# Optimization experiments

Measured on AMD Instinct MI355X. Metric: run time of the kernel, lower is better.

## Reference

```python
import jax, jax.numpy as jnp
import numpy as np

SR = 16000
HOP = 256
NH = 60
TWO_PI = 2.0 * np.pi


def _rescale(x):
    """Linear upsample along time (axis 1) by HOP, align_corners=True.
    x: [B, T, C] -> [B, T*HOP, C]. Matches F.interpolate(mode='linear', align_corners=True)."""
    T = x.shape[1]
    L = T * HOP
    pos = jnp.arange(L, dtype=jnp.float32) * (np.float32(T - 1) / np.float32(L - 1))
    i0 = jnp.clip(jnp.floor(pos).astype(jnp.int32), 0, T - 2)
    w = (pos - i0.astype(jnp.float32))[None, :, None]
    x0 = x[:, i0, :]
    x1 = x[:, i0 + 1, :]
    return x0 * (1.0 - w) + x1 * w


def setup_inputs() -> dict:
    key = jax.random.key(0)
    k1, k2, k3 = jax.random.split(key, 3)
    # fundamental frequency in a realistic 50-450 Hz range
    f0 = jax.random.uniform(k1, (8, 500, 1), dtype=jnp.float32) * 400.0 + 50.0
    loudness = jax.random.uniform(k2, (8, 500, 1), dtype=jnp.float32)
    harm_amps = jax.random.uniform(k3, (8, 500, NH), dtype=jnp.float32)
    return {"f0": f0, "loudness": loudness, "harm_amps": harm_amps}


def reference(f0, loudness, harm_amps):
    ks = jnp.arange(1, NH + 1, dtype=f0.dtype)          # harmonic numbers
    harmonics = f0 * ks                                  # [B,T,H] (einsum ijk,k->ijk with broadcast f0)
    harm_amps = jnp.where(harmonics > (SR // 2), 0.0, harm_amps)  # Nyquist mask
    harmonics = _rescale(harmonics * (TWO_PI / SR))      # [B, T*HOP, H] angular increments
    phases = jnp.mod(jnp.cumsum(harmonics, axis=1), TWO_PI)
    loud = _rescale(loudness)                            # [B, T*HOP, 1]
    amps = _rescale(harm_amps)                           # [B, T*HOP, H]
    signal = jnp.sum(loud * amps * jnp.sin(phases), axis=2)  # [B, T*HOP]
    return signal
```

## Files before the change

kernel.cpp:

```cpp
#include <hip/hip_runtime.h>
#include <hip/hip_bf16.h>


#define NHARM 60
#define TFRAMES 500
#define TM1 499
#define LOUT 128000
#define LM1U 127999u

__global__ __launch_bounds__(512) void osc_prefix_kernel(const float* __restrict__ f0,
                                                         double* __restrict__ H) {
    int b = blockIdx.x;
    int tid = threadIdx.x;
    double g = 0.0;
    if (tid < TM1) {
        unsigned t = (unsigned)tid;
        unsigned a   = (t * LM1U + 498u) / 499u;
        unsigned end = (t < TM1 - 1u) ? ((t + 1u) * LM1U + 498u) / 499u - 1u
                                      : LM1U;
        unsigned cnt   = end - a + 1u;
        unsigned rem_a = a * 499u - t * LM1U;
        unsigned num = cnt * rem_a + 499u * (cnt * (cnt - 1u) / 2u);
        double F = (double)num / 127999.0;
        double fa = (double)f0[b * TFRAMES + tid];
        double fb = (double)f0[b * TFRAMES + tid + 1];
        g = (double)cnt * fa + (fb - fa) * F;
    }
    __shared__ double sd[512];
    sd[tid] = g;
    __syncthreads();
    for (int off = 1; off < 512; off <<= 1) {
        double v = sd[tid];
        double o = (tid >= off) ? sd[tid - off] : 0.0;
        __syncthreads();
        sd[tid] = v + o;
        __syncthreads();
    }
    if (tid < TM1) H[b * TM1 + tid] = sd[tid] - g;
}

__global__ __launch_bounds__(256) void osc_main_kernel(const float* __restrict__ f0,
                                                       const float* __restrict__ loud,
                                                       const float* __restrict__ amps,
                                                       const double* __restrict__ H,
                                                       float* __restrict__ out) {
    const int b    = blockIdx.y;
    const int tid  = threadIdx.x;
    const int base = blockIdx.x * 512;
    const int n0   = base + 2 * tid;

    unsigned t0 = (unsigned)base * 499u / LM1U;
    if (t0 > 498u) t0 = 498u;
    __shared__ float2 sPair[3][64];
    if (tid < 192) {
        const int r = tid >> 6, c = tid & 63;
        if (c < NHARM) {
            const unsigned ra = min(t0 + (unsigned)r, 499u);
            const unsigned rb = min(ra + 1u, 499u);
            const float fa = f0[b * TFRAMES + ra];
            const float fb = f0[b * TFRAMES + rb];
            const float va = amps[((size_t)b * TFRAMES + ra) * NHARM + c];
            const float vb = amps[((size_t)b * TFRAMES + rb) * NHARM + c];
            const float kf = (float)(c + 1);
            sPair[r][c] = make_float2((fa * kf > 8000.f) ? 0.f : va,
                                      (fb * kf > 8000.f) ? 0.f : vb);
        }
    }
    __syncthreads();

    float phf[2], frw[2], lnv[2], fmn[2];
    const float2* pbase[2];
#pragma unroll
    for (int s = 0; s < 2; ++s) {
        const int n = n0 + s;
        unsigned p = (unsigned)n * 499u;
        unsigned t = p / LM1U;
        if (t > 498u) t = 498u;
        unsigned rem = p - t * LM1U;
        unsigned a = (t * LM1U + 498u) / 499u;
        unsigned rem_a = a * 499u - t * LM1U;
        unsigned cnt = (unsigned)n - a + 1u;
        unsigned num = cnt * rem_a + 499u * (cnt * (cnt - 1u) / 2u);
        double F = (double)num / 127999.0;

        const float f0a = f0[b * TFRAMES + t];
        const float f0b = f0[b * TFRAMES + t + 1];
        double U = (double)cnt * (double)f0a + ((double)f0b - (double)f0a) * F;
        double V = H[b * TM1 + t] + U;

        const float fracf = (float)rem * (1.0f / 127999.0f);
        const float la = loud[b * TFRAMES + t];
        const float lb = loud[b * TFRAMES + t + 1];

        const double rev1 = V * (1.0 / 16000.0);
        phf[s] = (float)(rev1 - floor(rev1));
        frw[s] = fracf;
        lnv[s] = la + fracf * (lb - la);
        fmn[s] = fminf(f0a, f0b);
        pbase[s] = &sPair[t - t0][0];
    }

    const int hm = min(NHARM, (int)(8000.0f / fminf(fmn[0], fmn[1])) + 1);

    const float2* __restrict__ p0 = pbase[0];
    const float2* __restrict__ p1 = pbase[1];
    float a0A = 0.f, a0B = 0.f, a1A = 0.f, a1B = 0.f;
#pragma unroll 4
    for (int h = 0; h < hm; ++h) {
        const float kf = (float)(h + 1);
        float r0 = phf[0] * kf; r0 -= floorf(r0);
        float r1 = phf[1] * kf; r1 -= floorf(r1);
        const float s0 = __builtin_amdgcn_sinf(r0);
        const float s1 = __builtin_amdgcn_sinf(r1);
        const float2 ab0 = p0[h];
        const float2 ab1 = p1[h];
        a0A += ab0.x * s0; a0B += ab0.y * s0;
        a1A += ab1.x * s1; a1B += ab1.y * s1;
    }
    const float acc0 = a0A + frw[0] * (a0B - a0A);
    const float acc1 = a1A + frw[1] * (a1B - a1A);
    float2 o = make_float2(acc0 * lnv[0], acc1 * lnv[1]);
    *reinterpret_cast<float2*>(&out[(size_t)b * LOUT + n0]) = o;
}

extern "C" void kernel_launch(void* const* d_in, const int* in_sizes, int n_in,
                              void* d_out, int out_size, void* d_ws, size_t ws_size,
                              hipStream_t stream) {
    const float* f0   = (const float*)d_in[0];
    const float* loud = (const float*)d_in[1];
    const float* amps = (const float*)d_in[2];
    double* H  = (double*)d_ws;
    float* out = (float*)d_out;

    osc_prefix_kernel<<<dim3(8), dim3(512), 0, stream>>>(f0, H);
    osc_main_kernel<<<dim3(250, 8), dim3(256), 0, stream>>>(f0, loud, amps, H, out);
}
```

Before: 75.02 us.

## Fuse phase prefix-sum into main oscillator kernel via per-block recomputation

Removes the separate prefix-scan kernel and its workspace round trip. Each block now recomputes the phase prefix up to its start frame with one wavefront, using a strided loop over frames and a shuffle reduction, while the other wavefronts load amplitudes. This drops one kernel launch and the dependency between two launches, but adds redundant double-precision work of up to about 500 frame totals per block.

```diff
diff --git a/kernel.cpp b/kernel.cpp
--- a/kernel.cpp
+++ b/kernel.cpp
@@ -4,46 +4,28 @@
 
 #define NHARM 60
 #define TFRAMES 500
-#define TM1 499
 #define LOUT 128000
 #define LM1U 127999u
+#define INV_LM1 (1.0 / 127999.0)
 
-__global__ __launch_bounds__(512) void osc_prefix_kernel(const float* __restrict__ f0,
-                                                         double* __restrict__ H) {
-    int b = blockIdx.x;
-    int tid = threadIdx.x;
-    double g = 0.0;
-    if (tid < TM1) {
-        unsigned t = (unsigned)tid;
-        unsigned a   = (t * LM1U + 498u) / 499u;
-        unsigned end = (t < TM1 - 1u) ? ((t + 1u) * LM1U + 498u) / 499u - 1u
-                                      : LM1U;
-        unsigned cnt   = end - a + 1u;
-        unsigned rem_a = a * 499u - t * LM1U;
-        unsigned num = cnt * rem_a + 499u * (cnt * (cnt - 1u) / 2u);
-        double F = (double)num / 127999.0;
-        double fa = (double)f0[b * TFRAMES + tid];
-        double fb = (double)f0[b * TFRAMES + tid + 1];
-        g = (double)cnt * fa + (fb - fa) * F;
-    }
-    __shared__ double sd[512];
-    sd[tid] = g;
-    __syncthreads();
-    for (int off = 1; off < 512; off <<= 1) {
-        double v = sd[tid];
-        double o = (tid >= off) ? sd[tid - off] : 0.0;
-        __syncthreads();
-        sd[tid] = v + o;
-        __syncthreads();
-    }
-    if (tid < TM1) H[b * TM1 + tid] = sd[tid] - g;
+__device__ __forceinline__ double frame_total(const float* __restrict__ f0,
+                                              int b, unsigned t) {
+    unsigned a   = (t * LM1U + 498u) / 499u;
+    unsigned end = (t < 498u) ? ((t + 1u) * LM1U + 498u) / 499u - 1u
+                              : LM1U;
+    unsigned cnt   = end - a + 1u;
+    unsigned rem_a = a * 499u - t * LM1U;
+    unsigned num = cnt * rem_a + 499u * (cnt * (cnt - 1u) / 2u);
+    double F = (double)num * INV_LM1;
+    double fa = (double)f0[b * TFRAMES + (int)t];
+    double fb = (double)f0[b * TFRAMES + (int)t + 1];
+    return (double)cnt * fa + (fb - fa) * F;
 }
 
-__global__ __launch_bounds__(256) void osc_main_kernel(const float* __restrict__ f0,
-                                                       const float* __restrict__ loud,
-                                                       const float* __restrict__ amps,
-                                                       const double* __restrict__ H,
-                                                       float* __restrict__ out) {
+__global__ __launch_bounds__(256) void osc_fused_kernel(const float* __restrict__ f0,
+                                                        const float* __restrict__ loud,
+                                                        const float* __restrict__ amps,
+                                                        float* __restrict__ out) {
     const int b    = blockIdx.y;
     const int tid  = threadIdx.x;
     const int base = blockIdx.x * 512;
@@ -51,9 +33,25 @@
 
     unsigned t0 = (unsigned)base * 499u / LM1U;
     if (t0 > 498u) t0 = 498u;
+
     __shared__ float2 sPair[3][64];
-    if (tid < 192) {
-        const int r = tid >> 6, c = tid & 63;
+    __shared__ double gsh[2];
+    __shared__ double Ssh;
+
+    if (tid < 64) {
+        const unsigned tlim = min(t0 + 2u, 499u);
+        double psum = 0.0;
+        for (unsigned tp = (unsigned)tid; tp < tlim; tp += 64u) {
+            const double g = frame_total(f0, b, tp);
+            if (tp < t0) psum += g;
+            else         gsh[tp - t0] = g;
+        }
+#pragma unroll
+        for (int off = 32; off > 0; off >>= 1)
+            psum += __shfl_down(psum, off, 64);
+        if (tid == 0) Ssh = psum;
+    } else if (tid < 256) {
+        const int r = (tid - 64) >> 6, c = (tid - 64) & 63;
         if (c < NHARM) {
             const unsigned ra = min(t0 + (unsigned)r, 499u);
             const unsigned rb = min(ra + 1u, 499u);
@@ -68,6 +66,10 @@
     }
     __syncthreads();
 
+    const double S  = Ssh;
+    const double g0 = gsh[0];
+    const double g1 = gsh[1];
+
     float phf[2], frw[2], lnv[2], fmn[2];
     const float2* pbase[2];
 #pragma unroll
@@ -81,12 +83,16 @@
         unsigned rem_a = a * 499u - t * LM1U;
         unsigned cnt = (unsigned)n - a + 1u;
         unsigned num = cnt * rem_a + 499u * (cnt * (cnt - 1u) / 2u);
-        double F = (double)num / 127999.0;
+        double F = (double)num * INV_LM1;
 
         const float f0a = f0[b * TFRAMES + t];
         const float f0b = f0[b * TFRAMES + t + 1];
         double U = (double)cnt * (double)f0a + ((double)f0b - (double)f0a) * F;
-        double V = H[b * TM1 + t] + U;
+        const unsigned r = t - t0;
+        double Hv = S;
+        if (r > 0u) Hv += g0;
+        if (r > 1u) Hv += g1;
+        double V = Hv + U;
 
         const float fracf = (float)rem * (1.0f / 127999.0f);
         const float la = loud[b * TFRAMES + t];
@@ -97,7 +103,7 @@
         frw[s] = fracf;
         lnv[s] = la + fracf * (lb - la);
         fmn[s] = fminf(f0a, f0b);
-        pbase[s] = &sPair[t - t0][0];
+        pbase[s] = &sPair[r][0];
     }
 
     const int hm = min(NHARM, (int)(8000.0f / fminf(fmn[0], fmn[1])) + 1);
@@ -129,9 +135,7 @@
     const float* f0   = (const float*)d_in[0];
     const float* loud = (const float*)d_in[1];
     const float* amps = (const float*)d_in[2];
-    double* H  = (double*)d_ws;
     float* out = (float*)d_out;
 
-    osc_prefix_kernel<<<dim3(8), dim3(512), 0, stream>>>(f0, H);
-    osc_main_kernel<<<dim3(250, 8), dim3(256), 0, stream>>>(f0, loud, amps, H, out);
+    osc_fused_kernel<<<dim3(250, 8), dim3(256), 0, stream>>>(f0, loud, amps, out);
 }
```

Result: no change. 74.58 us (-0.6%).
